# Performance work log

Measured on AMD Instinct MI355X. Metric: run time of the kernel, lower is better.

Reference implementation:

```python
import jax, jax.numpy as jnp
import numpy as np

VOCAB, E, HIDDEN = 100000, 64, (64, 128, 64)
B, T = 4096, 200


def setup_inputs() -> dict:
    key = jax.random.key(0)
    ks = jax.random.split(key, 12)
    # glorot-ish scales
    def glorot(k, shape):
        fan_in, fan_out = shape[0], shape[-1]
        s = jnp.sqrt(6.0 / (fan_in + fan_out))
        return jax.random.uniform(k, shape, jnp.float32, -s, s)
    return {
        "query": jax.random.randint(ks[0], (B,), 0, VOCAB),
        "keys": jax.random.randint(ks[1], (B, T), 0, VOCAB),
        "emb": glorot(ks[2], (VOCAB, E)),
        "att_w1": glorot(ks[3], (4 * E, 64)),
        "att_b1": jnp.zeros((64,), jnp.float32),
        "att_w2": glorot(ks[4], (64, 1)),
        "att_b2": jnp.zeros((1,), jnp.float32),
        "deep_w1": glorot(ks[5], (HIDDEN[0], HIDDEN[1])),
        "deep_b1": jnp.zeros((HIDDEN[1],), jnp.float32),
        "deep_w2": glorot(ks[6], (HIDDEN[1], HIDDEN[2])),
        "deep_b2": jnp.zeros((HIDDEN[2],), jnp.float32),
        "out_w": glorot(ks[7], (HIDDEN[2], 1)),
        "out_b": jnp.zeros((1,), jnp.float32),
    }


def reference(query, keys, emb, att_w1, att_b1, att_w2, att_b2,
              deep_w1, deep_b1, deep_w2, deep_b2, out_w, out_b):
    q = emb[query]                # [B, E]
    k = emb[keys]                 # [B, T, E]
    qe = jnp.broadcast_to(q[:, None, :], k.shape)  # [B, T, E]
    inter = jnp.concatenate([qe, k, qe - k, qe * k], axis=-1)  # [B, T, 4E]
    h = jax.nn.relu(inter @ att_w1 + att_b1)       # [B, T, 64]
    scores = (h @ att_w2 + att_b2)[..., 0]         # [B, T]
    w = jax.nn.softmax(scores, axis=-1)            # [B, T]
    interest = jnp.einsum("bt,bte->be", w, k)      # [B, E]
    d = jax.nn.relu(interest @ deep_w1 + deep_b1)
    d = jax.nn.relu(d @ deep_w2 + deep_b2)
    return jax.nn.sigmoid(d @ out_w + out_b)       # [B, 1]
```

## Files before the change

kernel.cpp:

```cpp
#include <hip/hip_runtime.h>

#define T 200
#define E 64
#define NTILE 13
#define TPAD 208
#define ROW 72
#define MB 16

typedef __bf16 bf16_t;
typedef __bf16 bf16x8 __attribute__((ext_vector_type(8)));
typedef float f32x4 __attribute__((ext_vector_type(4)));

__global__ __launch_bounds__(256) void prep_kernel(
    const int* __restrict__ query,
    const float* __restrict__ emb,
    const float* __restrict__ w1,
    const float* __restrict__ b1,
    uint4* __restrict__ wsM,
    float* __restrict__ wsU)
{
    __shared__ float sTmp[64 * 65];
    __shared__ __align__(16) float sQ[64];
    __shared__ float sUP[256];

    const int tid = threadIdx.x;
    const int b   = blockIdx.x;

    const int qi = query[b];
    if (tid < 16) ((float4*)sQ)[tid] = ((const float4*)(emb + (size_t)qi * E))[tid];
    __syncthreads();

    {
        const int j = tid & 63, ec = tid >> 6;
        float au = 0.f;
        #pragma unroll
        for (int eo = 0; eo < 16; ++eo) {
            const int e = ec * 16 + eo;
            const float w1a = w1[e * 64 + j];
            const float w1b = w1[(64 + e) * 64 + j];
            const float w1c = w1[(128 + e) * 64 + j];
            const float w1d = w1[(192 + e) * 64 + j];
            sTmp[e * 65 + j] = w1b - w1c + sQ[e] * w1d;
            au = fmaf(sQ[e], w1a + w1c, au);
        }
        sUP[tid] = au;
    }
    __syncthreads();
    if (tid < 64)
        wsU[(size_t)b * 64 + tid] = b1[tid] + sUP[tid] + sUP[64 + tid] + sUP[128 + tid] + sUP[192 + tid];

    #pragma unroll
    for (int c = tid; c < 512; c += 256) {
        const int f = c >> 6, l = c & 63;
        const int nt = f >> 1, h = f & 1;
        const int n = l & 15, quad = l >> 4;
        const int j2 = nt * 16 + n;
        const int e0 = h * 32 + quad * 8;
        union { bf16_t hh[8]; uint4 v; } u;
        #pragma unroll
        for (int s = 0; s < 8; ++s) u.hh[s] = (bf16_t)sTmp[(e0 + s) * 65 + j2];
        wsM[(size_t)b * 512 + c] = u.v;
    }
}

__global__ __launch_bounds__(256) void main_kernel(
    const int* __restrict__ keys,
    const float* __restrict__ emb,
    const uint4* __restrict__ wsM,
    const float* __restrict__ wsU,
    const float* __restrict__ w2,
    const float* __restrict__ b2,
    float* __restrict__ wsI)
{
    __shared__ __align__(16) bf16_t sK[TPAD * ROW];
    __shared__ __align__(16) float sU[64];
    __shared__ __align__(16) float sW2f[64];
    __shared__ float sWgt[256];
    __shared__ float sUP[256];
    __shared__ float sRed[8];

    const int tid  = threadIdx.x;
    const int lane = tid & 63;
    const int wid  = tid >> 6;
    const int b    = blockIdx.x;

    uint4 kr[8];
    #pragma unroll
    for (int c = 0; c < 8; ++c) kr[c] = make_uint4(0u, 0u, 0u, 0u);
    if (tid < T) {
        const int ki = keys[b * T + tid];
        const float4* kp = (const float4*)(emb + (size_t)ki * E);
        #pragma unroll
        for (int c = 0; c < 8; ++c) {
            const float4 x = kp[2 * c], y = kp[2 * c + 1];
            union { bf16_t h[8]; uint4 v; } u;
            u.h[0] = (bf16_t)x.x; u.h[1] = (bf16_t)x.y; u.h[2] = (bf16_t)x.z; u.h[3] = (bf16_t)x.w;
            u.h[4] = (bf16_t)y.x; u.h[5] = (bf16_t)y.y; u.h[6] = (bf16_t)y.z; u.h[7] = (bf16_t)y.w;
            kr[c] = u.v;
        }
    }
    if (tid < 16) ((float4*)sU)[tid] = ((const float4*)(wsU + (size_t)b * 64))[tid];
    else if (tid < 32) ((float4*)sW2f)[tid - 16] = ((const float4*)w2)[tid - 16];
    const float b2v = b2[0];

    bf16x8 bF[4][2];
    {
        const uint4* mp = wsM + (size_t)b * 512;
        #pragma unroll
        for (int nt = 0; nt < 4; ++nt)
            #pragma unroll
            for (int h = 0; h < 2; ++h) {
                union { uint4 v; bf16x8 f; } u;
                u.v = mp[(nt * 2 + h) * 64 + lane];
                bF[nt][h] = u.f;
            }
    }

    if (tid < TPAD) {
        uint4* dst = (uint4*)(sK + tid * ROW);
        #pragma unroll
        for (int c = 0; c < 8; ++c) dst[c] = kr[c];
    }
    __syncthreads();

    {
        const int n    = lane & 15;
        const int quad = lane >> 4;
        float uvv[4], w2v[4];
        #pragma unroll
        for (int nt = 0; nt < 4; ++nt) { uvv[nt] = sU[nt * 16 + n]; w2v[nt] = sW2f[nt * 16 + n]; }
        for (int mt = wid; mt < NTILE; mt += 4) {
            const bf16x8 a0 = *(const bf16x8*)&sK[(mt * 16 + n) * ROW + quad * 8];
            const bf16x8 a1 = *(const bf16x8*)&sK[(mt * 16 + n) * ROW + 32 + quad * 8];
            float s0 = 0.f, s1 = 0.f, s2 = 0.f, s3 = 0.f;
            #pragma unroll
            for (int nt = 0; nt < 4; ++nt) {
                f32x4 acc = { uvv[nt], uvv[nt], uvv[nt], uvv[nt] };
                acc = __builtin_amdgcn_mfma_f32_16x16x32_bf16(a0, bF[nt][0], acc, 0, 0, 0);
                acc = __builtin_amdgcn_mfma_f32_16x16x32_bf16(a1, bF[nt][1], acc, 0, 0, 0);
                s0 = fmaf(fmaxf(acc[0], 0.f), w2v[nt], s0);
                s1 = fmaf(fmaxf(acc[1], 0.f), w2v[nt], s1);
                s2 = fmaf(fmaxf(acc[2], 0.f), w2v[nt], s2);
                s3 = fmaf(fmaxf(acc[3], 0.f), w2v[nt], s3);
            }
            #pragma unroll
            for (int off = 1; off < 16; off <<= 1) {
                s0 += __shfl_xor(s0, off);
                s1 += __shfl_xor(s1, off);
                s2 += __shfl_xor(s2, off);
                s3 += __shfl_xor(s3, off);
            }
            if (n == 0) {
                const int base = mt * 16 + quad * 4;
                sWgt[base + 0] = s0;
                sWgt[base + 1] = s1;
                sWgt[base + 2] = s2;
                sWgt[base + 3] = s3;
            }
        }
    }
    __syncthreads();

    {
        const float score = (tid < T) ? (sWgt[tid] + b2v) : -1e30f;
        float m = score;
        #pragma unroll
        for (int off = 32; off > 0; off >>= 1) m = fmaxf(m, __shfl_xor(m, off));
        if (lane == 0) sRed[wid] = m;
        __syncthreads();
        const float gmax = fmaxf(fmaxf(sRed[0], sRed[1]), fmaxf(sRed[2], sRed[3]));
        const float p = (tid < T) ? __expf(score - gmax) : 0.f;
        float s = p;
        #pragma unroll
        for (int off = 32; off > 0; off >>= 1) s += __shfl_xor(s, off);
        if (lane == 0) sRed[4 + wid] = s;
        __syncthreads();
        const float gsum = sRed[4] + sRed[5] + sRed[6] + sRed[7];
        sWgt[tid] = p / gsum;
    }
    __syncthreads();

    {
        const int e = tid & 63, ch = tid >> 6;
        float a = 0.f;
        #pragma unroll 4
        for (int tt = 0; tt < 52; ++tt) {
            const int t = ch * 52 + tt;
            a = fmaf(sWgt[t], (float)sK[t * ROW + e], a);
        }
        sUP[tid] = a;
    }
    __syncthreads();
    if (tid < 64)
        wsI[(size_t)b * 64 + tid] = sUP[tid] + sUP[64 + tid] + sUP[128 + tid] + sUP[192 + tid];
}

__global__ __launch_bounds__(256) void mlp_kernel(
    const float* __restrict__ wsI,
    const float* __restrict__ dw1,
    const float* __restrict__ db1,
    const float* __restrict__ dw2,
    const float* __restrict__ db2,
    const float* __restrict__ ow,
    const float* __restrict__ ob,
    float* __restrict__ out,
    int B)
{
    __shared__ __align__(16) float sDW1[64 * 128];
    __shared__ __align__(16) float sDW2[128 * 64];
    __shared__ __align__(16) float sI[MB * 68];
    __shared__ __align__(16) float sH1[MB * 132];
    __shared__ __align__(16) float sH2[MB * 68];
    __shared__ float sB1[128];
    __shared__ float sB2[64];
    __shared__ float sOW[64];

    const int tid = threadIdx.x;
    const int b0  = blockIdx.x * MB;

    for (int i = tid; i < 2048; i += 256) ((float4*)sDW1)[i] = ((const float4*)dw1)[i];
    for (int i = tid; i < 2048; i += 256) ((float4*)sDW2)[i] = ((const float4*)dw2)[i];
    if (tid < 128) sB1[tid] = db1[tid];
    if (tid < 64) { sB2[tid] = db2[tid]; sOW[tid] = ow[tid]; }
    {
        const int bi = tid >> 4, e4 = (tid & 15) * 4;
        if (b0 + bi < B) {
            const float4 v = *(const float4*)(wsI + (size_t)(b0 + bi) * 64 + e4);
            *(float4*)&sI[bi * 68 + e4] = v;
        }
    }
    __syncthreads();

    {
        const int bi = tid >> 4, jb = tid & 15;
        float iv[64];
        #pragma unroll
        for (int e4 = 0; e4 < 16; ++e4) {
            const float4 v = *(const float4*)&sI[bi * 68 + e4 * 4];
            iv[e4 * 4 + 0] = v.x; iv[e4 * 4 + 1] = v.y; iv[e4 * 4 + 2] = v.z; iv[e4 * 4 + 3] = v.w;
        }
        float a[8];
        #pragma unroll
        for (int jj = 0; jj < 8; ++jj) a[jj] = sB1[jb * 8 + jj];
        #pragma unroll 8
        for (int e = 0; e < 64; ++e) {
            const float4 w0 = *(const float4*)&sDW1[e * 128 + jb * 8];
            const float4 w4 = *(const float4*)&sDW1[e * 128 + jb * 8 + 4];
            const float x = iv[e];
            a[0] = fmaf(x, w0.x, a[0]); a[1] = fmaf(x, w0.y, a[1]);
            a[2] = fmaf(x, w0.z, a[2]); a[3] = fmaf(x, w0.w, a[3]);
            a[4] = fmaf(x, w4.x, a[4]); a[5] = fmaf(x, w4.y, a[5]);
            a[6] = fmaf(x, w4.z, a[6]); a[7] = fmaf(x, w4.w, a[7]);
        }
        #pragma unroll
        for (int jj = 0; jj < 4; ++jj) {
            float4 v;
            v.x = fmaxf(a[0 + ((jj & 1) * 4 + (jj >> 1) * 0)], 0.f);
            (void)v;
        }
        float4 v0, v1;
        v0.x = fmaxf(a[0], 0.f); v0.y = fmaxf(a[1], 0.f); v0.z = fmaxf(a[2], 0.f); v0.w = fmaxf(a[3], 0.f);
        v1.x = fmaxf(a[4], 0.f); v1.y = fmaxf(a[5], 0.f); v1.z = fmaxf(a[6], 0.f); v1.w = fmaxf(a[7], 0.f);
        *(float4*)&sH1[bi * 132 + jb * 8] = v0;
        *(float4*)&sH1[bi * 132 + jb * 8 + 4] = v1;
    }
    __syncthreads();

    {
        const int bi = tid >> 4, obb = tid & 15;
        float a0 = sB2[obb * 4 + 0], a1 = sB2[obb * 4 + 1], a2 = sB2[obb * 4 + 2], a3 = sB2[obb * 4 + 3];
        #pragma unroll 4
        for (int i4 = 0; i4 < 32; ++i4) {
            const float4 hv = *(const float4*)&sH1[bi * 132 + i4 * 4];
            const float4 wv0 = *(const float4*)&sDW2[(i4 * 4 + 0) * 64 + obb * 4];
            const float4 wv1 = *(const float4*)&sDW2[(i4 * 4 + 1) * 64 + obb * 4];
            const float4 wv2 = *(const float4*)&sDW2[(i4 * 4 + 2) * 64 + obb * 4];
            const float4 wv3 = *(const float4*)&sDW2[(i4 * 4 + 3) * 64 + obb * 4];
            a0 = fmaf(hv.x, wv0.x, a0); a1 = fmaf(hv.x, wv0.y, a1);
            a2 = fmaf(hv.x, wv0.z, a2); a3 = fmaf(hv.x, wv0.w, a3);
            a0 = fmaf(hv.y, wv1.x, a0); a1 = fmaf(hv.y, wv1.y, a1);
            a2 = fmaf(hv.y, wv1.z, a2); a3 = fmaf(hv.y, wv1.w, a3);
            a0 = fmaf(hv.z, wv2.x, a0); a1 = fmaf(hv.z, wv2.y, a1);
            a2 = fmaf(hv.z, wv2.z, a2); a3 = fmaf(hv.z, wv2.w, a3);
            a0 = fmaf(hv.w, wv3.x, a0); a1 = fmaf(hv.w, wv3.y, a1);
            a2 = fmaf(hv.w, wv3.z, a2); a3 = fmaf(hv.w, wv3.w, a3);
        }
        float4 v;
        v.x = fmaxf(a0, 0.f); v.y = fmaxf(a1, 0.f); v.z = fmaxf(a2, 0.f); v.w = fmaxf(a3, 0.f);
        *(float4*)&sH2[bi * 68 + obb * 4] = v;
    }
    __syncthreads();

    if (tid < MB) {
        const int bi = tid;
        float a = 0.f;
        #pragma unroll 8
        for (int o = 0; o < 64; ++o) a = fmaf(sH2[bi * 68 + o], sOW[o], a);
        if (b0 + bi < B) out[b0 + bi] = 1.f / (1.f + __expf(-(a + ob[0])));
    }
}

__global__ __launch_bounds__(256, 3) void din_mono(
    const int* __restrict__ query,
    const int* __restrict__ keys,
    const float* __restrict__ embf,
    const float* __restrict__ w1,
    const float* __restrict__ b1,
    const float* __restrict__ w2,
    const float* __restrict__ b2,
    const float* __restrict__ dw1,
    const float* __restrict__ db1,
    const float* __restrict__ dw2,
    const float* __restrict__ db2,
    const float* __restrict__ ow,
    const float* __restrict__ ob,
    float* __restrict__ out)
{
    __shared__ __align__(16) char sRaw[256 * ROW * 2];
    __shared__ __align__(16) bf16_t sMt[64 * ROW];
    __shared__ float sU[64];
    __shared__ float sUP[256];
    __shared__ float sW2f[64];
    __shared__ float sWgt[256];
    __shared__ float sQf[64];
    __shared__ float sRed[8];
    __shared__ float sInt[64];
    __shared__ float sD1[128];
    __shared__ float sD2[64];

    const int tid  = threadIdx.x;
    const int lane = tid & 63;
    const int wid  = tid >> 6;
    const int b    = blockIdx.x;
    const float b2v = b2[0];

    uint4 kr[8];
    #pragma unroll
    for (int c = 0; c < 8; ++c) kr[c] = make_uint4(0u, 0u, 0u, 0u);
    if (tid < T) {
        const int ki = keys[b * T + tid];
        const float4* kp = (const float4*)(embf + (size_t)ki * E);
        #pragma unroll
        for (int c = 0; c < 8; ++c) {
            const float4 x = kp[2 * c], y = kp[2 * c + 1];
            union { bf16_t h[8]; uint4 v; } u;
            u.h[0] = (bf16_t)x.x; u.h[1] = (bf16_t)x.y; u.h[2] = (bf16_t)x.z; u.h[3] = (bf16_t)x.w;
            u.h[4] = (bf16_t)y.x; u.h[5] = (bf16_t)y.y; u.h[6] = (bf16_t)y.z; u.h[7] = (bf16_t)y.w;
            kr[c] = u.v;
        }
    }
    const int qi = query[b];
    if (tid < 16) ((float4*)sQf)[tid] = ((const float4*)(embf + (size_t)qi * E))[tid];
    if (tid < 64) sW2f[tid] = w2[tid];
    __syncthreads();

    {
        float* sTmp = (float*)sRaw;
        const int j = tid & 63, ec = tid >> 6;
        float au = 0.f;
        #pragma unroll
        for (int eo = 0; eo < 16; ++eo) {
            const int e = ec * 16 + eo;
            const float w1a = w1[e * 64 + j];
            const float w1b = w1[(64 + e) * 64 + j];
            const float w1c = w1[(128 + e) * 64 + j];
            const float w1d = w1[(192 + e) * 64 + j];
            sTmp[e * 65 + j] = w1b - w1c + sQf[e] * w1d;
            au = fmaf(sQf[e], w1a + w1c, au);
        }
        sUP[tid] = au;
    }
    __syncthreads();
    {
        const float* sTmp = (const float*)sRaw;
        const int e = tid & 63, jc = tid >> 6;
        #pragma unroll
        for (int jo = 0; jo < 16; ++jo) {
            const int j = jc * 16 + jo;
            sMt[j * ROW + e] = (bf16_t)sTmp[e * 65 + j];
        }
    }
    if (tid < 64) sU[tid] = b1[tid] + sUP[tid] + sUP[64 + tid] + sUP[128 + tid] + sUP[192 + tid];
    __syncthreads();

    bf16_t* sK = (bf16_t*)sRaw;
    {
        uint4* dst = (uint4*)(sK + tid * ROW);
        #pragma unroll
        for (int c = 0; c < 8; ++c) dst[c] = kr[c];
    }
    __syncthreads();

    {
        const int n    = lane & 15;
        const int quad = lane >> 4;
        float w2v[4], uv[4];
        bf16x8 bF[4][2];
        #pragma unroll
        for (int nt = 0; nt < 4; ++nt) {
            w2v[nt] = sW2f[nt * 16 + n];
            uv[nt]  = sU[nt * 16 + n];
            bF[nt][0] = *(const bf16x8*)&sMt[(nt * 16 + n) * ROW + quad * 8];
            bF[nt][1] = *(const bf16x8*)&sMt[(nt * 16 + n) * ROW + 32 + quad * 8];
        }
        #pragma unroll
        for (int i = 0; i < 4; ++i) {
            const int mt = wid * 4 + i;
            const bf16x8 a0 = *(const bf16x8*)&sK[(mt * 16 + n) * ROW + quad * 8];
            const bf16x8 a1 = *(const bf16x8*)&sK[(mt * 16 + n) * ROW + 32 + quad * 8];
            float s0 = 0.f, s1 = 0.f, s2 = 0.f, s3 = 0.f;
            #pragma unroll
            for (int nt = 0; nt < 4; ++nt) {
                f32x4 acc = { uv[nt], uv[nt], uv[nt], uv[nt] };
                acc = __builtin_amdgcn_mfma_f32_16x16x32_bf16(a0, bF[nt][0], acc, 0, 0, 0);
                acc = __builtin_amdgcn_mfma_f32_16x16x32_bf16(a1, bF[nt][1], acc, 0, 0, 0);
                s0 = fmaf(fmaxf(acc[0], 0.f), w2v[nt], s0);
                s1 = fmaf(fmaxf(acc[1], 0.f), w2v[nt], s1);
                s2 = fmaf(fmaxf(acc[2], 0.f), w2v[nt], s2);
                s3 = fmaf(fmaxf(acc[3], 0.f), w2v[nt], s3);
            }
            #pragma unroll
            for (int off = 1; off < 16; off <<= 1) {
                s0 += __shfl_xor(s0, off);
                s1 += __shfl_xor(s1, off);
                s2 += __shfl_xor(s2, off);
                s3 += __shfl_xor(s3, off);
            }
            if (n == 0) {
                const int base = mt * 16 + quad * 4;
                sWgt[base + 0] = s0;
                sWgt[base + 1] = s1;
                sWgt[base + 2] = s2;
                sWgt[base + 3] = s3;
            }
        }
    }
    __syncthreads();

    {
        const float score = (tid < T) ? (sWgt[tid] + b2v) : -1e30f;
        float m = score;
        #pragma unroll
        for (int off = 32; off > 0; off >>= 1) m = fmaxf(m, __shfl_xor(m, off));
        if (lane == 0) sRed[wid] = m;
        __syncthreads();
        const float gmax = fmaxf(fmaxf(sRed[0], sRed[1]), fmaxf(sRed[2], sRed[3]));
        const float p = (tid < T) ? __expf(score - gmax) : 0.f;
        float s = p;
        #pragma unroll
        for (int off = 32; off > 0; off >>= 1) s += __shfl_xor(s, off);
        if (lane == 0) sRed[4 + wid] = s;
        __syncthreads();
        const float gsum = sRed[4] + sRed[5] + sRed[6] + sRed[7];
        sWgt[tid] = p / gsum;
    }
    __syncthreads();

    {
        const int e = tid & 63, ch = tid >> 6;
        float a = 0.f;
        #pragma unroll 8
        for (int tt = 0; tt < 64; ++tt) {
            const int t = ch * 64 + tt;
            a = fmaf(sWgt[t], (float)sK[t * ROW + e], a);
        }
        sUP[tid] = a;
    }
    __syncthreads();
    if (tid < 64) sInt[tid] = sUP[tid] + sUP[64 + tid] + sUP[128 + tid] + sUP[192 + tid];
    __syncthreads();

    if (tid < 128) {
        float a = db1[tid];
        #pragma unroll 8
        for (int e = 0; e < 64; ++e) a = fmaf(sInt[e], dw1[e * 128 + tid], a);
        sD1[tid] = fmaxf(a, 0.f);
    }
    __syncthreads();
    if (tid < 64) {
        float a = db2[tid];
        #pragma unroll 8
        for (int i = 0; i < 128; ++i) a = fmaf(sD1[i], dw2[i * 64 + tid], a);
        sD2[tid] = fmaxf(a, 0.f);
    }
    __syncthreads();
    if (tid < 64) {
        float v = sD2[tid] * ow[tid];
        #pragma unroll
        for (int off = 32; off > 0; off >>= 1) v += __shfl_xor(v, off);
        if (tid == 0) out[b] = 1.f / (1.f + __expf(-(v + ob[0])));
    }
}

extern "C" void kernel_launch(void* const* d_in, const int* in_sizes, int n_in,
                              void* d_out, int out_size, void* d_ws, size_t ws_size,
                              hipStream_t stream) {
    const int*   query = (const int*)d_in[0];
    const int*   keys  = (const int*)d_in[1];
    const float* embf  = (const float*)d_in[2];
    const float* w1    = (const float*)d_in[3];
    const float* b1    = (const float*)d_in[4];
    const float* w2    = (const float*)d_in[5];
    const float* b2    = (const float*)d_in[6];
    const float* dw1   = (const float*)d_in[7];
    const float* db1   = (const float*)d_in[8];
    const float* dw2   = (const float*)d_in[9];
    const float* db2   = (const float*)d_in[10];
    const float* ow    = (const float*)d_in[11];
    const float* ob    = (const float*)d_in[12];
    float* out = (float*)d_out;
    const int B = in_sizes[0];

    const size_t needM = (size_t)B * 8192;
    const size_t needU = (size_t)B * 256;
    const size_t needI = (size_t)B * 256;
    if (ws_size >= needM + needU + needI) {
        uint4* wsM = (uint4*)d_ws;
        float* wsU = (float*)((char*)d_ws + needM);
        float* wsI = (float*)((char*)d_ws + needM + needU);
        prep_kernel<<<B, 256, 0, stream>>>(query, embf, w1, b1, wsM, wsU);
        main_kernel<<<B, 256, 0, stream>>>(keys, embf, wsM, wsU, w2, b2, wsI);
        mlp_kernel<<<(B + MB - 1) / MB, 256, 0, stream>>>(wsI, dw1, db1, dw2, db2, ow, ob, out, B);
    } else {
        din_mono<<<B, 256, 0, stream>>>(query, keys, embf, w1, b1, w2, b2,
                                        dw1, db1, dw2, db2, ow, ob, out);
    }
}
```

Baseline: 175.5 us.

## Replace per-batch folded W1 prep with shared weights and in-kernel q*k MFMA

Instead of building a per-batch folded bf16 weight matrix (q folded into W1) in a B-block prep kernel and writing 8KB per row to workspace, a single-block setup kernel builds batch-independent bf16 matrices (W1b-W1c and W1d) plus W1a+W1c. The main kernel computes the q-dependent bias itself, forms q*k elementwise in registers, and issues twice as many MFMAs per tile. Key embedding gathers are also reorganised into coalesced 16-lane row loads via shared key indices. This removes the large per-batch workspace traffic and a full-grid kernel at the cost of doubled MFMA work and extra bf16 rounding of q*k.

```diff
diff --git a/kernel.cpp b/kernel.cpp
--- a/kernel.cpp
+++ b/kernel.cpp
@@ -11,133 +11,141 @@
 typedef __bf16 bf16x8 __attribute__((ext_vector_type(8)));
 typedef float f32x4 __attribute__((ext_vector_type(4)));
 
-__global__ __launch_bounds__(256) void prep_kernel(
-    const int* __restrict__ query,
-    const float* __restrict__ emb,
+__global__ __launch_bounds__(256) void setup_kernel(
     const float* __restrict__ w1,
-    const float* __restrict__ b1,
-    uint4* __restrict__ wsM,
-    float* __restrict__ wsU)
+    uint4* __restrict__ wsB,
+    float* __restrict__ wsAC)
 {
-    __shared__ float sTmp[64 * 65];
-    __shared__ __align__(16) float sQ[64];
-    __shared__ float sUP[256];
-
     const int tid = threadIdx.x;
-    const int b   = blockIdx.x;
-
-    const int qi = query[b];
-    if (tid < 16) ((float4*)sQ)[tid] = ((const float4*)(emb + (size_t)qi * E))[tid];
-    __syncthreads();
-
-    {
-        const int j = tid & 63, ec = tid >> 6;
-        float au = 0.f;
-        #pragma unroll
-        for (int eo = 0; eo < 16; ++eo) {
-            const int e = ec * 16 + eo;
-            const float w1a = w1[e * 64 + j];
-            const float w1b = w1[(64 + e) * 64 + j];
-            const float w1c = w1[(128 + e) * 64 + j];
-            const float w1d = w1[(192 + e) * 64 + j];
-            sTmp[e * 65 + j] = w1b - w1c + sQ[e] * w1d;
-            au = fmaf(sQ[e], w1a + w1c, au);
-        }
-        sUP[tid] = au;
-    }
-    __syncthreads();
-    if (tid < 64)
-        wsU[(size_t)b * 64 + tid] = b1[tid] + sUP[tid] + sUP[64 + tid] + sUP[128 + tid] + sUP[192 + tid];
-
-    #pragma unroll
     for (int c = tid; c < 512; c += 256) {
         const int f = c >> 6, l = c & 63;
         const int nt = f >> 1, h = f & 1;
         const int n = l & 15, quad = l >> 4;
-        const int j2 = nt * 16 + n;
+        const int j = nt * 16 + n;
         const int e0 = h * 32 + quad * 8;
-        union { bf16_t hh[8]; uint4 v; } u;
-        #pragma unroll
-        for (int s = 0; s < 8; ++s) u.hh[s] = (bf16_t)sTmp[(e0 + s) * 65 + j2];
-        wsM[(size_t)b * 512 + c] = u.v;
+        union { bf16_t hh[8]; uint4 v; } a, d;
+        #pragma unroll
+        for (int s = 0; s < 8; ++s) {
+            const int e = e0 + s;
+            a.hh[s] = (bf16_t)(w1[(64 + e) * 64 + j] - w1[(128 + e) * 64 + j]);
+            d.hh[s] = (bf16_t)(w1[(192 + e) * 64 + j]);
+        }
+        wsB[c] = a.v;
+        wsB[512 + c] = d.v;
+    }
+    for (int i = tid; i < 4096; i += 256) {
+        const int e = i >> 6, j = i & 63;
+        wsAC[i] = w1[e * 64 + j] + w1[(128 + e) * 64 + j];
     }
 }
 
 __global__ __launch_bounds__(256) void main_kernel(
+    const int* __restrict__ query,
     const int* __restrict__ keys,
     const float* __restrict__ emb,
-    const uint4* __restrict__ wsM,
-    const float* __restrict__ wsU,
+    const uint4* __restrict__ wsB,
+    const float* __restrict__ wsAC,
+    const float* __restrict__ b1,
     const float* __restrict__ w2,
     const float* __restrict__ b2,
     float* __restrict__ wsI)
 {
     __shared__ __align__(16) bf16_t sK[TPAD * ROW];
-    __shared__ __align__(16) float sU[64];
+    __shared__ __align__(16) float sQf[64];
     __shared__ __align__(16) float sW2f[64];
+    __shared__ float sU[64];
+    __shared__ float sUP[256];
     __shared__ float sWgt[256];
-    __shared__ float sUP[256];
     __shared__ float sRed[8];
+    __shared__ int sKeys[TPAD];
 
     const int tid  = threadIdx.x;
     const int lane = tid & 63;
     const int wid  = tid >> 6;
     const int b    = blockIdx.x;
-
-    uint4 kr[8];
+    const float b2v = b2[0];
+
+    if (tid < 16) ((float4*)sQf)[tid] = ((const float4*)(emb + (size_t)query[b] * E))[tid];
+    if (tid < T) sKeys[tid] = keys[b * T + tid];
+    else if (tid < TPAD) sKeys[tid] = -1;
+    if (tid < 64) sW2f[tid] = w2[tid];
+    __syncthreads();
+
+    {
+        const int l16  = tid & 15;
+        const int rsel = tid >> 4;
+        #pragma unroll
+        for (int it = 0; it < 13; ++it) {
+            const int row = it * 16 + rsel;
+            const int ki  = sKeys[row];
+            ushort4 v = make_ushort4(0, 0, 0, 0);
+            if (ki >= 0) {
+                const float4 x = ((const float4*)(emb + (size_t)ki * E))[l16];
+                union { bf16_t h[4]; ushort4 u; } c;
+                c.h[0] = (bf16_t)x.x; c.h[1] = (bf16_t)x.y;
+                c.h[2] = (bf16_t)x.z; c.h[3] = (bf16_t)x.w;
+                v = c.u;
+            }
+            *(ushort4*)&sK[row * ROW + l16 * 4] = v;
+        }
+    }
+
+    {
+        const int j = tid & 63, ec = tid >> 6;
+        float au = 0.f;
+        #pragma unroll
+        for (int eo = 0; eo < 16; ++eo) {
+            const int e = ec * 16 + eo;
+            au = fmaf(sQf[e], wsAC[e * 64 + j], au);
+        }
+        sUP[tid] = au;
+    }
+    __syncthreads();
+    if (tid < 64) sU[tid] = b1[tid] + sUP[tid] + sUP[64 + tid] + sUP[128 + tid] + sUP[192 + tid];
+
+    bf16x8 bN[4][2], bD[4][2];
     #pragma unroll
-    for (int c = 0; c < 8; ++c) kr[c] = make_uint4(0u, 0u, 0u, 0u);
-    if (tid < T) {
-        const int ki = keys[b * T + tid];
-        const float4* kp = (const float4*)(emb + (size_t)ki * E);
-        #pragma unroll
-        for (int c = 0; c < 8; ++c) {
-            const float4 x = kp[2 * c], y = kp[2 * c + 1];
-            union { bf16_t h[8]; uint4 v; } u;
-            u.h[0] = (bf16_t)x.x; u.h[1] = (bf16_t)x.y; u.h[2] = (bf16_t)x.z; u.h[3] = (bf16_t)x.w;
-            u.h[4] = (bf16_t)y.x; u.h[5] = (bf16_t)y.y; u.h[6] = (bf16_t)y.z; u.h[7] = (bf16_t)y.w;
-            kr[c] = u.v;
-        }
-    }
-    if (tid < 16) ((float4*)sU)[tid] = ((const float4*)(wsU + (size_t)b * 64))[tid];
-    else if (tid < 32) ((float4*)sW2f)[tid - 16] = ((const float4*)w2)[tid - 16];
-    const float b2v = b2[0];
-
-    bf16x8 bF[4][2];
-    {
-        const uint4* mp = wsM + (size_t)b * 512;
-        #pragma unroll
-        for (int nt = 0; nt < 4; ++nt)
-            #pragma unroll
-            for (int h = 0; h < 2; ++h) {
-                union { uint4 v; bf16x8 f; } u;
-                u.v = mp[(nt * 2 + h) * 64 + lane];
-                bF[nt][h] = u.f;
-            }
-    }
-
-    if (tid < TPAD) {
-        uint4* dst = (uint4*)(sK + tid * ROW);
-        #pragma unroll
-        for (int c = 0; c < 8; ++c) dst[c] = kr[c];
-    }
+    for (int nt = 0; nt < 4; ++nt)
+        #pragma unroll
+        for (int h = 0; h < 2; ++h) {
+            union { uint4 v; bf16x8 f; } u1, u2;
+            u1.v = wsB[(nt * 2 + h) * 64 + lane];
+            u2.v = wsB[512 + (nt * 2 + h) * 64 + lane];
+            bN[nt][h] = u1.f;
+            bD[nt][h] = u2.f;
+        }
     __syncthreads();
 
     {
         const int n    = lane & 15;
         const int quad = lane >> 4;
+        float qf0[8], qf1[8];
+        #pragma unroll
+        for (int j = 0; j < 8; ++j) {
+            qf0[j] = sQf[quad * 8 + j];
+            qf1[j] = sQf[32 + quad * 8 + j];
+        }
         float uvv[4], w2v[4];
         #pragma unroll
         for (int nt = 0; nt < 4; ++nt) { uvv[nt] = sU[nt * 16 + n]; w2v[nt] = sW2f[nt * 16 + n]; }
+
         for (int mt = wid; mt < NTILE; mt += 4) {
-            const bf16x8 a0 = *(const bf16x8*)&sK[(mt * 16 + n) * ROW + quad * 8];
-            const bf16x8 a1 = *(const bf16x8*)&sK[(mt * 16 + n) * ROW + 32 + quad * 8];
+            union { bf16x8 f; bf16_t h[8]; } a0, a1, a2, a3;
+            a0.f = *(const bf16x8*)&sK[(mt * 16 + n) * ROW + quad * 8];
+            a1.f = *(const bf16x8*)&sK[(mt * 16 + n) * ROW + 32 + quad * 8];
+            #pragma unroll
+            for (int j = 0; j < 8; ++j) {
+                a2.h[j] = (bf16_t)((float)a0.h[j] * qf0[j]);
+                a3.h[j] = (bf16_t)((float)a1.h[j] * qf1[j]);
+            }
             float s0 = 0.f, s1 = 0.f, s2 = 0.f, s3 = 0.f;
             #pragma unroll
             for (int nt = 0; nt < 4; ++nt) {
                 f32x4 acc = { uvv[nt], uvv[nt], uvv[nt], uvv[nt] };
-                acc = __builtin_amdgcn_mfma_f32_16x16x32_bf16(a0, bF[nt][0], acc, 0, 0, 0);
-                acc = __builtin_amdgcn_mfma_f32_16x16x32_bf16(a1, bF[nt][1], acc, 0, 0, 0);
+                acc = __builtin_amdgcn_mfma_f32_16x16x32_bf16(a0.f, bN[nt][0], acc, 0, 0, 0);
+                acc = __builtin_amdgcn_mfma_f32_16x16x32_bf16(a1.f, bN[nt][1], acc, 0, 0, 0);
+                acc = __builtin_amdgcn_mfma_f32_16x16x32_bf16(a2.f, bD[nt][0], acc, 0, 0, 0);
+                acc = __builtin_amdgcn_mfma_f32_16x16x32_bf16(a3.f, bD[nt][1], acc, 0, 0, 0);
                 s0 = fmaf(fmaxf(acc[0], 0.f), w2v[nt], s0);
                 s1 = fmaf(fmaxf(acc[1], 0.f), w2v[nt], s1);
                 s2 = fmaf(fmaxf(acc[2], 0.f), w2v[nt], s2);
@@ -251,12 +259,6 @@
             a[2] = fmaf(x, w0.z, a[2]); a[3] = fmaf(x, w0.w, a[3]);
             a[4] = fmaf(x, w4.x, a[4]); a[5] = fmaf(x, w4.y, a[5]);
             a[6] = fmaf(x, w4.z, a[6]); a[7] = fmaf(x, w4.w, a[7]);
-        }
-        #pragma unroll
-        for (int jj = 0; jj < 4; ++jj) {
-            float4 v;
-            v.x = fmaxf(a[0 + ((jj & 1) * 4 + (jj >> 1) * 0)], 0.f);
-            (void)v;
         }
         float4 v0, v1;
         v0.x = fmaxf(a[0], 0.f); v0.y = fmaxf(a[1], 0.f); v0.z = fmaxf(a[2], 0.f); v0.w = fmaxf(a[3], 0.f);
@@ -511,15 +513,15 @@
     float* out = (float*)d_out;
     const int B = in_sizes[0];
 
-    const size_t needM = (size_t)B * 8192;
-    const size_t needU = (size_t)B * 256;
-    const size_t needI = (size_t)B * 256;
-    if (ws_size >= needM + needU + needI) {
-        uint4* wsM = (uint4*)d_ws;
-        float* wsU = (float*)((char*)d_ws + needM);
-        float* wsI = (float*)((char*)d_ws + needM + needU);
-        prep_kernel<<<B, 256, 0, stream>>>(query, embf, w1, b1, wsM, wsU);
-        main_kernel<<<B, 256, 0, stream>>>(keys, embf, wsM, wsU, w2, b2, wsI);
+    const size_t needB  = 1024 * sizeof(uint4);
+    const size_t needAC = 4096 * sizeof(float);
+    const size_t needI  = (size_t)B * 64 * sizeof(float);
+    if (ws_size >= needB + needAC + needI) {
+        uint4* wsB  = (uint4*)d_ws;
+        float* wsAC = (float*)((char*)d_ws + needB);
+        float* wsI  = (float*)((char*)d_ws + needB + needAC);
+        setup_kernel<<<1, 256, 0, stream>>>(w1, wsB, wsAC);
+        main_kernel<<<B, 256, 0, stream>>>(query, keys, embf, wsB, wsAC, b1, w2, b2, wsI);
         mlp_kernel<<<(B + MB - 1) / MB, 256, 0, stream>>>(wsI, dw1, db1, dw2, db2, ow, ob, out, B);
     } else {
         din_mono<<<B, 256, 0, stream>>>(query, keys, embf, w1, b1, w2, b2,
```

Result: slower. 189.0 us (+7.7%).

## Precompute query-independent W1 combinations once and batch prep over 16 queries

Applied to the files above, without the earlier changes.

Adds a single-block setup kernel that computes the query-independent W1 combinations (w1b-w1c, w1d, w1a+w1c) into workspace tables in the MMA fragment order. The per-query prep kernel becomes a 16-query-per-block kernel that stages these tables in shared memory and reuses them across the batch, instead of re-reading and re-combining all of W1 for every query. This cuts redundant global reads and block count in the prep stage, but adds an extra serialized single-block launch and larger shared-memory use per block, which lowers occupancy. Dead code in the MLP kernel is also removed.

```diff
diff --git a/kernel.cpp b/kernel.cpp
--- a/kernel.cpp
+++ b/kernel.cpp
@@ -6,60 +6,106 @@
 #define TPAD 208
 #define ROW 72
 #define MB 16
+#define PB 16
 
 typedef __bf16 bf16_t;
 typedef __bf16 bf16x8 __attribute__((ext_vector_type(8)));
 typedef float f32x4 __attribute__((ext_vector_type(4)));
 
-__global__ __launch_bounds__(256) void prep_kernel(
-    const int* __restrict__ query,
-    const float* __restrict__ emb,
+__global__ __launch_bounds__(256) void setup_kernel(
     const float* __restrict__ w1,
-    const float* __restrict__ b1,
-    uint4* __restrict__ wsM,
-    float* __restrict__ wsU)
+    float* __restrict__ wsN1f,
+    float* __restrict__ wsDf,
+    float* __restrict__ wsACf)
 {
-    __shared__ float sTmp[64 * 65];
-    __shared__ __align__(16) float sQ[64];
-    __shared__ float sUP[256];
-
     const int tid = threadIdx.x;
-    const int b   = blockIdx.x;
-
-    const int qi = query[b];
-    if (tid < 16) ((float4*)sQ)[tid] = ((const float4*)(emb + (size_t)qi * E))[tid];
-    __syncthreads();
-
-    {
-        const int j = tid & 63, ec = tid >> 6;
-        float au = 0.f;
-        #pragma unroll
-        for (int eo = 0; eo < 16; ++eo) {
-            const int e = ec * 16 + eo;
-            const float w1a = w1[e * 64 + j];
-            const float w1b = w1[(64 + e) * 64 + j];
-            const float w1c = w1[(128 + e) * 64 + j];
-            const float w1d = w1[(192 + e) * 64 + j];
-            sTmp[e * 65 + j] = w1b - w1c + sQ[e] * w1d;
-            au = fmaf(sQ[e], w1a + w1c, au);
-        }
-        sUP[tid] = au;
-    }
-    __syncthreads();
-    if (tid < 64)
-        wsU[(size_t)b * 64 + tid] = b1[tid] + sUP[tid] + sUP[64 + tid] + sUP[128 + tid] + sUP[192 + tid];
-
-    #pragma unroll
     for (int c = tid; c < 512; c += 256) {
         const int f = c >> 6, l = c & 63;
         const int nt = f >> 1, h = f & 1;
         const int n = l & 15, quad = l >> 4;
-        const int j2 = nt * 16 + n;
+        const int j = nt * 16 + n;
         const int e0 = h * 32 + quad * 8;
-        union { bf16_t hh[8]; uint4 v; } u;
-        #pragma unroll
-        for (int s = 0; s < 8; ++s) u.hh[s] = (bf16_t)sTmp[(e0 + s) * 65 + j2];
-        wsM[(size_t)b * 512 + c] = u.v;
+        #pragma unroll
+        for (int s = 0; s < 8; ++s) {
+            const int e = e0 + s;
+            wsN1f[c * 8 + s] = w1[(64 + e) * 64 + j] - w1[(128 + e) * 64 + j];
+            wsDf[c * 8 + s]  = w1[(192 + e) * 64 + j];
+        }
+    }
+    for (int i = tid; i < 4096; i += 256) {
+        const int e = i >> 6, j = i & 63;
+        wsACf[i] = w1[e * 64 + j] + w1[(128 + e) * 64 + j];
+    }
+}
+
+__global__ __launch_bounds__(256) void prep2_kernel(
+    const int* __restrict__ query,
+    const float* __restrict__ emb,
+    const float* __restrict__ wsN1f,
+    const float* __restrict__ wsDf,
+    const float* __restrict__ wsACf,
+    const float* __restrict__ b1,
+    uint4* __restrict__ wsM,
+    float* __restrict__ wsU,
+    int B)
+{
+    __shared__ __align__(16) float sN1[4096];
+    __shared__ __align__(16) float sD[4096];
+    __shared__ __align__(16) float sAC[4096];
+    __shared__ __align__(16) float sQ[PB * 64];
+    __shared__ float sB1v[64];
+
+    const int tid = threadIdx.x;
+    const int b0  = blockIdx.x * PB;
+
+    for (int i = tid; i < 1024; i += 256) ((float4*)sN1)[i] = ((const float4*)wsN1f)[i];
+    for (int i = tid; i < 1024; i += 256) ((float4*)sD)[i]  = ((const float4*)wsDf)[i];
+    for (int i = tid; i < 1024; i += 256) ((float4*)sAC)[i] = ((const float4*)wsACf)[i];
+    if (tid < 64) sB1v[tid] = b1[tid];
+    {
+        const int ib = tid >> 4, l16 = tid & 15;
+        float4 v = make_float4(0.f, 0.f, 0.f, 0.f);
+        if (b0 + ib < B)
+            v = ((const float4*)(emb + (size_t)query[b0 + ib] * E))[l16];
+        ((float4*)&sQ[ib * 64])[l16] = v;
+    }
+    __syncthreads();
+
+    {
+        const int j = tid & 63, grp = tid >> 6;
+        for (int ib = grp; ib < PB; ib += 4) {
+            if (b0 + ib >= B) break;
+            float u = sB1v[j];
+            const float* q = &sQ[ib * 64];
+            #pragma unroll 8
+            for (int e = 0; e < 64; ++e) u = fmaf(q[e], sAC[e * 64 + j], u);
+            wsU[(size_t)(b0 + ib) * 64 + j] = u;
+        }
+    }
+
+    #pragma unroll
+    for (int k = 0; k < 2; ++k) {
+        const int c = tid + k * 256;
+        const int f = c >> 6, l = c & 63;
+        const int e0 = (f & 1) * 32 + (l >> 4) * 8;
+        const float4 n1a = ((const float4*)sN1)[c * 2];
+        const float4 n1b = ((const float4*)sN1)[c * 2 + 1];
+        const float4 da  = ((const float4*)sD)[c * 2];
+        const float4 db  = ((const float4*)sD)[c * 2 + 1];
+        for (int ib = 0; ib < PB; ++ib) {
+            if (b0 + ib >= B) break;
+            const float* q = &sQ[ib * 64 + e0];
+            union { bf16_t h[8]; uint4 v; } u;
+            u.h[0] = (bf16_t)(n1a.x + q[0] * da.x);
+            u.h[1] = (bf16_t)(n1a.y + q[1] * da.y);
+            u.h[2] = (bf16_t)(n1a.z + q[2] * da.z);
+            u.h[3] = (bf16_t)(n1a.w + q[3] * da.w);
+            u.h[4] = (bf16_t)(n1b.x + q[4] * db.x);
+            u.h[5] = (bf16_t)(n1b.y + q[5] * db.y);
+            u.h[6] = (bf16_t)(n1b.z + q[6] * db.z);
+            u.h[7] = (bf16_t)(n1b.w + q[7] * db.w);
+            wsM[(size_t)(b0 + ib) * 512 + c] = u.v;
+        }
     }
 }
 
@@ -251,12 +297,6 @@
             a[2] = fmaf(x, w0.z, a[2]); a[3] = fmaf(x, w0.w, a[3]);
             a[4] = fmaf(x, w4.x, a[4]); a[5] = fmaf(x, w4.y, a[5]);
             a[6] = fmaf(x, w4.z, a[6]); a[7] = fmaf(x, w4.w, a[7]);
-        }
-        #pragma unroll
-        for (int jj = 0; jj < 4; ++jj) {
-            float4 v;
-            v.x = fmaxf(a[0 + ((jj & 1) * 4 + (jj >> 1) * 0)], 0.f);
-            (void)v;
         }
         float4 v0, v1;
         v0.x = fmaxf(a[0], 0.f); v0.y = fmaxf(a[1], 0.f); v0.z = fmaxf(a[2], 0.f); v0.w = fmaxf(a[3], 0.f);
@@ -511,14 +551,20 @@
     float* out = (float*)d_out;
     const int B = in_sizes[0];
 
-    const size_t needM = (size_t)B * 8192;
-    const size_t needU = (size_t)B * 256;
-    const size_t needI = (size_t)B * 256;
-    if (ws_size >= needM + needU + needI) {
-        uint4* wsM = (uint4*)d_ws;
-        float* wsU = (float*)((char*)d_ws + needM);
-        float* wsI = (float*)((char*)d_ws + needM + needU);
-        prep_kernel<<<B, 256, 0, stream>>>(query, embf, w1, b1, wsM, wsU);
+    const size_t needTab = 3 * 4096 * sizeof(float);
+    const size_t needM   = (size_t)B * 512 * sizeof(uint4);
+    const size_t needU   = (size_t)B * 64 * sizeof(float);
+    const size_t needI   = (size_t)B * 64 * sizeof(float);
+    if (ws_size >= needTab + needM + needU + needI) {
+        float* wsN1f = (float*)d_ws;
+        float* wsDf  = wsN1f + 4096;
+        float* wsACf = wsDf + 4096;
+        uint4* wsM   = (uint4*)((char*)d_ws + needTab);
+        float* wsU   = (float*)((char*)d_ws + needTab + needM);
+        float* wsI   = wsU + (size_t)B * 64;
+        setup_kernel<<<1, 256, 0, stream>>>(w1, wsN1f, wsDf, wsACf);
+        prep2_kernel<<<(B + PB - 1) / PB, 256, 0, stream>>>(query, embf, wsN1f, wsDf, wsACf,
+                                                            b1, wsM, wsU, B);
         main_kernel<<<B, 256, 0, stream>>>(keys, embf, wsM, wsU, w2, b2, wsI);
         mlp_kernel<<<(B + MB - 1) / MB, 256, 0, stream>>>(wsI, dw1, db1, dw2, db2, ow, ob, out, B);
     } else {
```

Measured after the change: 177.3 us. No clear change (+1.0%).
